# Kernel optimization log

Hardware: AMD Instinct MI355X
Metric: run time of the kernel (lower is better)

## Reference

```python
import jax, jax.numpy as jnp
import numpy as np

N_AGENTS = 8
STATE_DIM = 256
EMBED_DIM = 32
BATCH = 65536


def setup_inputs() -> dict:
    key = jax.random.key(0)
    ks = jax.random.split(key, 12)
    s = 1.0 / np.sqrt(STATE_DIM)
    se = 1.0 / np.sqrt(EMBED_DIM)
    return {
        "agent_qs": jax.random.normal(ks[0], (BATCH, N_AGENTS), dtype=jnp.float32),
        "states": jax.random.normal(ks[1], (BATCH, STATE_DIM), dtype=jnp.float32),
        # hyper_w_1: Linear(state_dim, embed_dim * n_agents)
        "w1_W": jax.random.uniform(ks[2], (STATE_DIM, EMBED_DIM * N_AGENTS), jnp.float32, -s, s),
        "w1_b": jax.random.uniform(ks[3], (EMBED_DIM * N_AGENTS,), jnp.float32, -s, s),
        # hyper_w_final: Linear(state_dim, embed_dim)
        "wf_W": jax.random.uniform(ks[4], (STATE_DIM, EMBED_DIM), jnp.float32, -s, s),
        "wf_b": jax.random.uniform(ks[5], (EMBED_DIM,), jnp.float32, -s, s),
        # hyper_b_1: Linear(state_dim, embed_dim)
        "b1_W": jax.random.uniform(ks[6], (STATE_DIM, EMBED_DIM), jnp.float32, -s, s),
        "b1_b": jax.random.uniform(ks[7], (EMBED_DIM,), jnp.float32, -s, s),
        # V: Linear(state_dim, embed_dim) -> ReLU -> Linear(embed_dim, 1)
        "v1_W": jax.random.uniform(ks[8], (STATE_DIM, EMBED_DIM), jnp.float32, -s, s),
        "v1_b": jax.random.uniform(ks[9], (EMBED_DIM,), jnp.float32, -s, s),
        "v2_W": jax.random.uniform(ks[10], (EMBED_DIM, 1), jnp.float32, -se, se),
        "v2_b": jax.random.uniform(ks[11], (1,), jnp.float32, -se, se),
    }


def reference(agent_qs, states, w1_W, w1_b, wf_W, wf_b, b1_W, b1_b, v1_W, v1_b, v2_W, v2_b):
    B = agent_qs.shape[0]
    # hypernet weights (abs for monotonicity)
    w1 = jnp.abs(states @ w1_W + w1_b).reshape(B, N_AGENTS, EMBED_DIM)   # [B, A, E]
    w_final = jnp.abs(states @ wf_W + wf_b)                               # [B, E]
    b1 = states @ b1_W + b1_b                                             # [B, E]
    # hidden = elu(agent_qs^T w1 + b1): [B,1,A] @ [B,A,E] -> [B,E]
    hidden = jax.nn.elu(jnp.einsum("ba,bae->be", agent_qs, w1) + b1)
    # mixed = hidden @ w_final: [B,1,E] @ [B,E,1] -> [B,1]
    mixed = jnp.sum(hidden * w_final, axis=-1, keepdims=True)             # [B, 1]
    # state value V(s)
    state_value = jax.nn.relu(states @ v1_W + v1_b) @ v2_W + v2_b         # [B, 1]
    return mixed + state_value
```

## Files before the change

kernel.cpp:

```cpp
#include <hip/hip_runtime.h>
#include <math.h>


#define NTILES 22
#define KCHUNKS 8
#define CHUNK_I4 1408

typedef __attribute__((ext_vector_type(8))) short short8;
typedef __attribute__((ext_vector_type(4))) float float4v;

__device__ __forceinline__ unsigned short f2b(float f) {
    unsigned int u = __float_as_uint(f);
    u = u + 0x7fffu + ((u >> 16) & 1u);
    return (unsigned short)(u >> 16);
}

__device__ __forceinline__ void gl2lds16(const unsigned short* g, unsigned short* l) {
    __builtin_amdgcn_global_load_lds(
        (const __attribute__((address_space(1))) unsigned int*)g,
        (__attribute__((address_space(3))) unsigned int*)l,
        16, 0, 0);
}

__global__ void repack_b(const float* __restrict__ w1_W,
                         const float* __restrict__ wf_W,
                         const float* __restrict__ b1_W,
                         const float* __restrict__ v1_W,
                         unsigned short* __restrict__ brep) {
    int idx = blockIdx.x * 256 + threadIdx.x;
    int lane = idx & 63;
    int tt   = idx >> 6;
    int t    = tt % 22;
    int kc   = tt / 22;
    int kbase = kc * 32 + (lane >> 4) * 8;
    int n = t * 16 + (lane & 15);
    short8 frag;
#pragma unroll
    for (int j = 0; j < 8; ++j) {
        int k = kbase + j;
        float val;
        if (n < 256)      val = w1_W[k * 256 + n];
        else if (n < 288) val = wf_W[k * 32 + (n - 256)];
        else if (n < 320) val = b1_W[k * 32 + (n - 288)];
        else              val = v1_W[k * 32 + (n - 320)];
        frag[j] = (short)f2b(val);
    }
    *(short8*)(&brep[idx * 8]) = frag;
}

__global__ void __launch_bounds__(256, 3)
qmix_main(const float* __restrict__ agent_qs,
          const float* __restrict__ states,
          const unsigned short* __restrict__ brep,
          const float* __restrict__ w1_b,
          const float* __restrict__ wf_b,
          const float* __restrict__ b1_b,
          const float* __restrict__ v1_b,
          const float* __restrict__ v2_W,
          const float* __restrict__ v2_b,
          float* __restrict__ out) {
    __shared__ __align__(16) unsigned short wlds[2][NTILES * 64 * 8];

    const int tid  = threadIdx.x;
    const int wave = tid >> 6, lane = tid & 63;
    const int quad = lane >> 4, l16 = lane & 15;
    const int row  = blockIdx.x * 64 + wave * 16 + l16;
    const float* srow = states + (size_t)row * 256;

    for (int s = wave; s < NTILES; s += 4)
        gl2lds16(brep + (size_t)(s * 64 + lane) * 8, wlds[0] + s * 512);

    float4v s0a = *(const float4v*)(srow + quad * 8);
    float4v s0b = *(const float4v*)(srow + quad * 8 + 4);

    float4v acc[NTILES];
#pragma unroll
    for (int t = 0; t < NTILES; ++t)
#pragma unroll
        for (int q = 0; q < 4; ++q) acc[t][q] = 0.f;

    __syncthreads();

    int cur = 0;
    for (int kc = 0; kc < KCHUNKS; ++kc) {
        if (kc < KCHUNKS - 1) {
            const unsigned short* src = brep + (size_t)(kc + 1) * CHUNK_I4 * 8;
            unsigned short* dst = wlds[cur ^ 1];
            for (int s = wave; s < NTILES; s += 4)
                gl2lds16(src + (size_t)(s * 64 + lane) * 8, dst + s * 512);
        }
        short8 b0;
#pragma unroll
        for (int j = 0; j < 4; ++j) {
            b0[j] = (short)f2b(s0a[j]); b0[4 + j] = (short)f2b(s0b[j]);
        }
        if (kc < KCHUNKS - 1) {
            const float* p0 = srow + (kc + 1) * 32 + quad * 8;
            s0a = *(const float4v*)(p0);
            s0b = *(const float4v*)(p0 + 4);
        }
        const short8* wb = (const short8*)wlds[cur] + lane;
#pragma unroll
        for (int t = 0; t < NTILES; ++t) {
            short8 af = wb[t * 64];
            acc[t] = __builtin_amdgcn_mfma_f32_16x16x32_bf16(af, b0, acc[t], 0, 0, 0);
        }
        cur ^= 1;
        __syncthreads();
    }

    float4v q0 = *(const float4v*)(agent_qs + (size_t)row * 8);
    float4v q1 = *(const float4v*)(agent_qs + (size_t)row * 8 + 4);
    float qv[8] = {q0[0], q0[1], q0[2], q0[3], q1[0], q1[1], q1[2], q1[3]};

    float qacc[8], wfv[8], b1v[8], svp = 0.f;
#pragma unroll
    for (int s = 0; s < 8; ++s) qacc[s] = 0.f;

#pragma unroll
    for (int t = 0; t < NTILES; ++t) {
        const float* bptr =
            (t < 16) ? (w1_b + t * 16) :
            (t < 18) ? (wf_b + (t - 16) * 16) :
            (t < 20) ? (b1_b + (t - 18) * 16) : (v1_b + (t - 20) * 16);
        float4v bb = *(const float4v*)(bptr + quad * 4);
        float vb[4];
#pragma unroll
        for (int j = 0; j < 4; ++j) vb[j] = acc[t][j] + bb[j];

        if (t < 16) {
            float q = qv[t >> 1];
            int base = (t & 1) * 4;
#pragma unroll
            for (int j = 0; j < 4; ++j) qacc[base + j] += q * fabsf(vb[j]);
        } else if (t < 18) {
            int base = (t - 16) * 4;
#pragma unroll
            for (int j = 0; j < 4; ++j) wfv[base + j] = fabsf(vb[j]);
        } else if (t < 20) {
            int base = (t - 18) * 4;
#pragma unroll
            for (int j = 0; j < 4; ++j) b1v[base + j] = vb[j];
        } else {
            int ebase = (t - 20) * 16 + quad * 4;
#pragma unroll
            for (int j = 0; j < 4; ++j)
                svp += fmaxf(vb[j], 0.f) * v2_W[ebase + j];
        }
    }

    float mix = 0.f;
#pragma unroll
    for (int s = 0; s < 8; ++s) {
        float h = qacc[s] + b1v[s];
        h = h > 0.f ? h : (__expf(h) - 1.f);
        mix += h * wfv[s];
    }
    float tot = mix + svp;
    tot += __shfl_xor(tot, 16);
    tot += __shfl_xor(tot, 32);
    if (quad == 0) out[row] = tot + v2_b[0];
}

extern "C" void kernel_launch(void* const* d_in, const int* in_sizes, int n_in,
                              void* d_out, int out_size, void* d_ws, size_t ws_size,
                              hipStream_t stream) {
    const float* agent_qs = (const float*)d_in[0];
    const float* states   = (const float*)d_in[1];
    const float* w1_W = (const float*)d_in[2];
    const float* w1_b = (const float*)d_in[3];
    const float* wf_W = (const float*)d_in[4];
    const float* wf_b = (const float*)d_in[5];
    const float* b1_W = (const float*)d_in[6];
    const float* b1_b = (const float*)d_in[7];
    const float* v1_W = (const float*)d_in[8];
    const float* v1_b = (const float*)d_in[9];
    const float* v2_W = (const float*)d_in[10];
    const float* v2_b = (const float*)d_in[11];
    float* out = (float*)d_out;
    unsigned short* brep = (unsigned short*)d_ws;

    repack_b<<<44, 256, 0, stream>>>(w1_W, wf_W, b1_W, v1_W, brep);
    qmix_main<<<1024, 256, 0, stream>>>(agent_qs, states, brep,
                                        w1_b, wf_b, b1_b, v1_b, v2_W, v2_b, out);
}
```

Before: 143.4 us.

## Keep most weight tiles resident in LDS and loop blocks over row tiles

Weight fragments are re-laid out so 19 of the 22 column tiles, across all K chunks, sit in LDS, loaded once per block. The remaining 3 tiles are streamed from global memory into registers with double buffering. Each block now processes 4 row tiles of 64 rows, so the grid shrinks to 256 blocks and the per-chunk double-buffered LDS reload and its barriers disappear. In exchange, LDS per block is larger (about 152 KB) and occupancy drops to 2 blocks per launch bound, and only 256 blocks are launched, which may underfill the GPU.

```diff
diff --git a/kernel.cpp b/kernel.cpp
--- a/kernel.cpp
+++ b/kernel.cpp
@@ -4,7 +4,9 @@
 
 #define NTILES 22
 #define KCHUNKS 8
-#define CHUNK_I4 1408
+#define LDS_TILES 19
+#define LDS_SLOTS (LDS_TILES * KCHUNKS)
+#define ROWTILES 4
 
 typedef __attribute__((ext_vector_type(8))) short short8;
 typedef __attribute__((ext_vector_type(4))) float float4v;
@@ -29,9 +31,10 @@
                          unsigned short* __restrict__ brep) {
     int idx = blockIdx.x * 256 + threadIdx.x;
     int lane = idx & 63;
-    int tt   = idx >> 6;
-    int t    = tt % 22;
-    int kc   = tt / 22;
+    int slot = idx >> 6;
+    int t, kc;
+    if (slot < LDS_SLOTS) { t = slot >> 3; kc = slot & 7; }
+    else { int r = slot - LDS_SLOTS; kc = r / 3; t = LDS_TILES + r % 3; }
     int kbase = kc * 32 + (lane >> 4) * 8;
     int n = t * 16 + (lane & 15);
     short8 frag;
@@ -48,7 +51,7 @@
     *(short8*)(&brep[idx * 8]) = frag;
 }
 
-__global__ void __launch_bounds__(256, 3)
+__global__ void __launch_bounds__(256, 2)
 qmix_main(const float* __restrict__ agent_qs,
           const float* __restrict__ states,
           const unsigned short* __restrict__ brep,
@@ -59,107 +62,115 @@
           const float* __restrict__ v2_W,
           const float* __restrict__ v2_b,
           float* __restrict__ out) {
-    __shared__ __align__(16) unsigned short wlds[2][NTILES * 64 * 8];
+    __shared__ __align__(16) unsigned short wlds[LDS_SLOTS * 512];
 
     const int tid  = threadIdx.x;
     const int wave = tid >> 6, lane = tid & 63;
     const int quad = lane >> 4, l16 = lane & 15;
-    const int row  = blockIdx.x * 64 + wave * 16 + l16;
-    const float* srow = states + (size_t)row * 256;
 
-    for (int s = wave; s < NTILES; s += 4)
-        gl2lds16(brep + (size_t)(s * 64 + lane) * 8, wlds[0] + s * 512);
-
-    float4v s0a = *(const float4v*)(srow + quad * 8);
-    float4v s0b = *(const float4v*)(srow + quad * 8 + 4);
-
-    float4v acc[NTILES];
-#pragma unroll
-    for (int t = 0; t < NTILES; ++t)
-#pragma unroll
-        for (int q = 0; q < 4; ++q) acc[t][q] = 0.f;
-
+    for (int s = wave; s < LDS_SLOTS; s += 4)
+        gl2lds16(brep + (size_t)(s * 64 + lane) * 8, wlds + s * 512);
     __syncthreads();
 
-    int cur = 0;
-    for (int kc = 0; kc < KCHUNKS; ++kc) {
-        if (kc < KCHUNKS - 1) {
-            const unsigned short* src = brep + (size_t)(kc + 1) * CHUNK_I4 * 8;
-            unsigned short* dst = wlds[cur ^ 1];
-            for (int s = wave; s < NTILES; s += 4)
-                gl2lds16(src + (size_t)(s * 64 + lane) * 8, dst + s * 512);
+    const short8* wl = (const short8*)wlds + lane;
+    const short8* ws = (const short8*)brep + LDS_SLOTS * 64 + lane;
+
+    for (int tt = 0; tt < ROWTILES; ++tt) {
+        const int row = blockIdx.x * (ROWTILES * 64) + tt * 64 + wave * 16 + l16;
+        const float* srow = states + (size_t)row * 256;
+
+        float4v s0a = *(const float4v*)(srow + quad * 8);
+        float4v s0b = *(const float4v*)(srow + quad * 8 + 4);
+        short8 sf[2][3];
+#pragma unroll
+        for (int u = 0; u < 3; ++u) sf[0][u] = ws[u * 64];
+
+        float4v acc[NTILES];
+#pragma unroll
+        for (int t = 0; t < NTILES; ++t)
+#pragma unroll
+            for (int q = 0; q < 4; ++q) acc[t][q] = 0.f;
+
+#pragma unroll
+        for (int kc = 0; kc < KCHUNKS; ++kc) {
+            if (kc + 1 < KCHUNKS) {
+#pragma unroll
+                for (int u = 0; u < 3; ++u)
+                    sf[(kc + 1) & 1][u] = ws[((kc + 1) * 3 + u) * 64];
+            }
+            short8 b0;
+#pragma unroll
+            for (int j = 0; j < 4; ++j) {
+                b0[j] = (short)f2b(s0a[j]); b0[4 + j] = (short)f2b(s0b[j]);
+            }
+            if (kc + 1 < KCHUNKS) {
+                const float* p0 = srow + (kc + 1) * 32 + quad * 8;
+                s0a = *(const float4v*)(p0);
+                s0b = *(const float4v*)(p0 + 4);
+            }
+#pragma unroll
+            for (int t = 0; t < LDS_TILES; ++t) {
+                short8 af = wl[(t * 8 + kc) * 64];
+                acc[t] = __builtin_amdgcn_mfma_f32_16x16x32_bf16(af, b0, acc[t], 0, 0, 0);
+            }
+#pragma unroll
+            for (int u = 0; u < 3; ++u)
+                acc[LDS_TILES + u] = __builtin_amdgcn_mfma_f32_16x16x32_bf16(
+                    sf[kc & 1][u], b0, acc[LDS_TILES + u], 0, 0, 0);
         }
-        short8 b0;
+
+        float4v q0 = *(const float4v*)(agent_qs + (size_t)row * 8);
+        float4v q1 = *(const float4v*)(agent_qs + (size_t)row * 8 + 4);
+        float qv[8] = {q0[0], q0[1], q0[2], q0[3], q1[0], q1[1], q1[2], q1[3]};
+
+        float qacc[8], wfv[8], b1v[8], svp = 0.f;
 #pragma unroll
-        for (int j = 0; j < 4; ++j) {
-            b0[j] = (short)f2b(s0a[j]); b0[4 + j] = (short)f2b(s0b[j]);
-        }
-        if (kc < KCHUNKS - 1) {
-            const float* p0 = srow + (kc + 1) * 32 + quad * 8;
-            s0a = *(const float4v*)(p0);
-            s0b = *(const float4v*)(p0 + 4);
-        }
-        const short8* wb = (const short8*)wlds[cur] + lane;
+        for (int s = 0; s < 8; ++s) qacc[s] = 0.f;
+
 #pragma unroll
         for (int t = 0; t < NTILES; ++t) {
-            short8 af = wb[t * 64];
-            acc[t] = __builtin_amdgcn_mfma_f32_16x16x32_bf16(af, b0, acc[t], 0, 0, 0);
+            const float* bptr =
+                (t < 16) ? (w1_b + t * 16) :
+                (t < 18) ? (wf_b + (t - 16) * 16) :
+                (t < 20) ? (b1_b + (t - 18) * 16) : (v1_b + (t - 20) * 16);
+            float4v bb = *(const float4v*)(bptr + quad * 4);
+            float vb[4];
+#pragma unroll
+            for (int j = 0; j < 4; ++j) vb[j] = acc[t][j] + bb[j];
+
+            if (t < 16) {
+                float q = qv[t >> 1];
+                int base = (t & 1) * 4;
+#pragma unroll
+                for (int j = 0; j < 4; ++j) qacc[base + j] += q * fabsf(vb[j]);
+            } else if (t < 18) {
+                int base = (t - 16) * 4;
+#pragma unroll
+                for (int j = 0; j < 4; ++j) wfv[base + j] = fabsf(vb[j]);
+            } else if (t < 20) {
+                int base = (t - 18) * 4;
+#pragma unroll
+                for (int j = 0; j < 4; ++j) b1v[base + j] = vb[j];
+            } else {
+                int ebase = (t - 20) * 16 + quad * 4;
+#pragma unroll
+                for (int j = 0; j < 4; ++j)
+                    svp += fmaxf(vb[j], 0.f) * v2_W[ebase + j];
+            }
         }
-        cur ^= 1;
-        __syncthreads();
+
+        float mix = 0.f;
+#pragma unroll
+        for (int s = 0; s < 8; ++s) {
+            float h = qacc[s] + b1v[s];
+            h = h > 0.f ? h : (__expf(h) - 1.f);
+            mix += h * wfv[s];
+        }
+        float tot = mix + svp;
+        tot += __shfl_xor(tot, 16);
+        tot += __shfl_xor(tot, 32);
+        if (quad == 0) out[row] = tot + v2_b[0];
     }
-
-    float4v q0 = *(const float4v*)(agent_qs + (size_t)row * 8);
-    float4v q1 = *(const float4v*)(agent_qs + (size_t)row * 8 + 4);
-    float qv[8] = {q0[0], q0[1], q0[2], q0[3], q1[0], q1[1], q1[2], q1[3]};
-
-    float qacc[8], wfv[8], b1v[8], svp = 0.f;
-#pragma unroll
-    for (int s = 0; s < 8; ++s) qacc[s] = 0.f;
-
-#pragma unroll
-    for (int t = 0; t < NTILES; ++t) {
-        const float* bptr =
-            (t < 16) ? (w1_b + t * 16) :
-            (t < 18) ? (wf_b + (t - 16) * 16) :
-            (t < 20) ? (b1_b + (t - 18) * 16) : (v1_b + (t - 20) * 16);
-        float4v bb = *(const float4v*)(bptr + quad * 4);
-        float vb[4];
-#pragma unroll
-        for (int j = 0; j < 4; ++j) vb[j] = acc[t][j] + bb[j];
-
-        if (t < 16) {
-            float q = qv[t >> 1];
-            int base = (t & 1) * 4;
-#pragma unroll
-            for (int j = 0; j < 4; ++j) qacc[base + j] += q * fabsf(vb[j]);
-        } else if (t < 18) {
-            int base = (t - 16) * 4;
-#pragma unroll
-            for (int j = 0; j < 4; ++j) wfv[base + j] = fabsf(vb[j]);
-        } else if (t < 20) {
-            int base = (t - 18) * 4;
-#pragma unroll
-            for (int j = 0; j < 4; ++j) b1v[base + j] = vb[j];
-        } else {
-            int ebase = (t - 20) * 16 + quad * 4;
-#pragma unroll
-            for (int j = 0; j < 4; ++j)
-                svp += fmaxf(vb[j], 0.f) * v2_W[ebase + j];
-        }
-    }
-
-    float mix = 0.f;
-#pragma unroll
-    for (int s = 0; s < 8; ++s) {
-        float h = qacc[s] + b1v[s];
-        h = h > 0.f ? h : (__expf(h) - 1.f);
-        mix += h * wfv[s];
-    }
-    float tot = mix + svp;
-    tot += __shfl_xor(tot, 16);
-    tot += __shfl_xor(tot, 32);
-    if (quad == 0) out[row] = tot + v2_b[0];
 }
 
 extern "C" void kernel_launch(void* const* d_in, const int* in_sizes, int n_in,
@@ -181,6 +192,6 @@
     unsigned short* brep = (unsigned short*)d_ws;
 
     repack_b<<<44, 256, 0, stream>>>(w1_W, wf_W, b1_W, v1_W, brep);
-    qmix_main<<<1024, 256, 0, stream>>>(agent_qs, states, brep,
-                                        w1_b, wf_b, b1_b, v1_b, v2_W, v2_b, out);
+    qmix_main<<<256, 256, 0, stream>>>(agent_qs, states, brep,
+                                       w1_b, wf_b, b1_b, v1_b, v2_W, v2_b, out);
 }
```

Measured after the change: 303.1 us. 111% more time.
